# Kernel tuning notes

Hardware: AMD Instinct MI355X
Metric: run time of the kernel (lower is better)

The kernel has to match this reference:

```python
import jax, jax.numpy as jnp
import numpy as np

U = 128          # uniform segment extent (operand_extent)
NSEG = 32        # segments per operand (in0, in1, out)
NPATH = 512      # number of paths
BATCH = 2048


def setup_inputs() -> dict:
    key = jax.random.key(0)
    k0, k1, kc, kp0, kp1, kpo = jax.random.split(key, 6)
    x0 = jax.random.normal(k0, (BATCH, NSEG * U), dtype=jnp.float32)
    x1 = jax.random.normal(k1, (BATCH, NSEG * U), dtype=jnp.float32)
    coeffs = jax.random.normal(kc, (NPATH,), dtype=jnp.float32)
    p0 = jax.random.randint(kp0, (NPATH,), 0, NSEG, dtype=jnp.int32)
    p1 = jax.random.randint(kp1, (NPATH,), 0, NSEG, dtype=jnp.int32)
    pout = jax.random.randint(kpo, (NPATH,), 0, NSEG, dtype=jnp.int32)
    return {"x0": x0, "x1": x1, "coeffs": coeffs, "p0": p0, "p1": p1, "pout": pout}


def reference(x0, x1, coeffs, p0, p1, pout):
    # Segmented uniform tensor product, subscripts 'u,u,u':
    # out[b, pout[k], :] += coeffs[k] * x0[b, p0[k], :] * x1[b, p1[k], :]
    B = x0.shape[0]
    x0s = x0.reshape(B, NSEG, U)
    x1s = x1.reshape(B, NSEG, U)
    # gather per-path segments: [B, P, U]
    contrib = x0s[:, p0, :] * x1s[:, p1, :] * coeffs[None, :, None]
    out = jnp.zeros((B, NSEG, U), dtype=x0.dtype).at[:, pout, :].add(contrib)
    return out.reshape(B, NSEG * U)
```

## Files before the change

### kernel.cpp

```cpp
#include <hip/hip_runtime.h>

#define U 128
#define NSEG 32
#define NPATH 512
#define ROW (NSEG * U)
#define NW 8

struct Meta { unsigned pp; float c; };
struct WS {
    Meta meta[NPATH];
    int  segstart[NSEG + 1];
    int  wsplit[NW + 1];
};

__global__ __launch_bounds__(512) void build_csr(const float* __restrict__ coeffs,
                                                 const int* __restrict__ p0,
                                                 const int* __restrict__ p1,
                                                 const int* __restrict__ pout,
                                                 WS* __restrict__ ws) {
    __shared__ int wcnt[NPATH / 64][NSEG];
    __shared__ int wpre[NPATH / 64][NSEG];
    __shared__ int sseg[NSEG + 1];
    __shared__ int stot[NSEG];

    const int k    = threadIdx.x;
    const int lane = k & 63;
    const int wave = k >> 6;

    const int   po = pout[k];
    const int   a0 = p0[k];
    const int   a1 = p1[k];
    const float c  = coeffs[k];

    const unsigned long long lt = (1ull << lane) - 1ull;
    int rank = 0;
    #pragma unroll
    for (int s = 0; s < NSEG; ++s) {
        unsigned long long m = __ballot(po == s);
        if (po == s)  rank = (int)__popcll(m & lt);
        if (lane == s) wcnt[wave][s] = (int)__popcll(m);
    }
    __syncthreads();

    if (k < NSEG) {
        int tot = 0;
        #pragma unroll
        for (int w = 0; w < NPATH / 64; ++w) { wpre[w][k] = tot; tot += wcnt[w][k]; }
        stot[k] = tot;
    }
    __syncthreads();

    if (k < 64) {
        int v = (k < NSEG) ? stot[k] : 0;
        int inc = v;
        #pragma unroll
        for (int d = 1; d < 64; d <<= 1) {
            int t = __shfl_up(inc, d, 64);
            if (k >= d) inc += t;
        }
        int excl = inc - v;
        if (k < NSEG) sseg[k] = excl;
        if (k == NSEG - 1) sseg[NSEG] = excl + v;
    }
    __syncthreads();

    {
        Meta m;
        m.pp = (unsigned)a0 | ((unsigned)a1 << 16);
        m.c  = c;
        ws->meta[sseg[po] + wpre[wave][po] + rank] = m;
    }
    if (k <= NSEG) ws->segstart[k] = sseg[k];

    if (k < 64) {
        #pragma unroll
        for (int w = 1; w < NW; ++w) {
            const int target = (NPATH * w) / NW;
            int key;
            if (k <= NSEG) {
                int d = sseg[k] - target; if (d < 0) d = -d;
                key = (d << 6) | k;
            } else key = 0x7fffffff;
            #pragma unroll
            for (int m = 32; m >= 1; m >>= 1) {
                int o = __shfl_xor(key, m, 64);
                key = (o < key) ? o : key;
            }
            if (k == 0) ws->wsplit[w] = key & 63;
        }
        if (k == 0) { ws->wsplit[0] = 0; ws->wsplit[NW] = NSEG; }
    }
}

__global__ __launch_bounds__(512) void tp_kernel(const float* __restrict__ x0,
                                                 const float* __restrict__ x1,
                                                 const WS* __restrict__ ws,
                                                 float* __restrict__ out) {
    __shared__ float lds0[ROW];
    __shared__ float lds1[ROW];
    __shared__ Meta  smeta[NPATH];
    __shared__ int   sseg[NSEG + 1];
    __shared__ int   ssplit[NW + 1];

    const int b   = blockIdx.x;
    const int tid = threadIdx.x;

    const float4* g0 = reinterpret_cast<const float4*>(x0 + (size_t)b * ROW);
    const float4* g1 = reinterpret_cast<const float4*>(x1 + (size_t)b * ROW);
    float4* s0v = reinterpret_cast<float4*>(lds0);
    float4* s1v = reinterpret_cast<float4*>(lds1);
    #pragma unroll
    for (int j = 0; j < (ROW / 4) / 512; ++j) {
        s0v[tid + j * 512] = g0[tid + j * 512];
        s1v[tid + j * 512] = g1[tid + j * 512];
    }
    if (tid < NPATH / 2)
        reinterpret_cast<float4*>(smeta)[tid] =
            reinterpret_cast<const float4*>(ws->meta)[tid];
    if (tid < NSEG + 1) sseg[tid] = ws->segstart[tid];
    if (tid < NW + 1)   ssplit[tid] = ws->wsplit[tid];
    __syncthreads();

    const int wave = tid >> 6;
    const int lane = tid & 63;
    const int half = lane >> 5;
    const int sub  = lane & 31;

    const int sBeg = __builtin_amdgcn_readfirstlane(ssplit[wave]);
    const int sEnd = __builtin_amdgcn_readfirstlane(ssplit[wave + 1]);

    const float4* s0q = reinterpret_cast<const float4*>(lds0);
    const float4* s1q = reinterpret_cast<const float4*>(lds1);
    float* outrow = out + (size_t)b * ROW;

    for (int s = sBeg; s < sEnd; ++s) {
        const int jb = __builtin_amdgcn_readfirstlane(sseg[s]);
        const int je = __builtin_amdgcn_readfirstlane(sseg[s + 1]);
        float4 acc0 = make_float4(0.f, 0.f, 0.f, 0.f);
        float4 acc1 = make_float4(0.f, 0.f, 0.f, 0.f);
        int j = jb;
        for (; j + 3 < je; j += 4) {
            const Meta mA = smeta[j + half];
            const Meta mB = smeta[j + 2 + half];
            const float4 uA = s0q[(mA.pp & 0xffffu) * (U / 4) + sub];
            const float4 wA = s1q[(mA.pp >> 16)     * (U / 4) + sub];
            const float4 uB = s0q[(mB.pp & 0xffffu) * (U / 4) + sub];
            const float4 wB = s1q[(mB.pp >> 16)     * (U / 4) + sub];
            acc0.x += mA.c * uA.x * wA.x;
            acc0.y += mA.c * uA.y * wA.y;
            acc0.z += mA.c * uA.z * wA.z;
            acc0.w += mA.c * uA.w * wA.w;
            acc1.x += mB.c * uB.x * wB.x;
            acc1.y += mB.c * uB.y * wB.y;
            acc1.z += mB.c * uB.z * wB.z;
            acc1.w += mB.c * uB.w * wB.w;
        }
        for (; j + 1 < je; j += 2) {
            const Meta m = smeta[j + half];
            const float4 u = s0q[(m.pp & 0xffffu) * (U / 4) + sub];
            const float4 w = s1q[(m.pp >> 16)     * (U / 4) + sub];
            acc0.x += m.c * u.x * w.x;
            acc0.y += m.c * u.y * w.y;
            acc0.z += m.c * u.z * w.z;
            acc0.w += m.c * u.w * w.w;
        }
        if (j < je) {
            const Meta m = smeta[j];
            const float cc = (half == 0) ? m.c : 0.f;
            const float4 u = s0q[(m.pp & 0xffffu) * (U / 4) + sub];
            const float4 w = s1q[(m.pp >> 16)     * (U / 4) + sub];
            acc0.x += cc * u.x * w.x;
            acc0.y += cc * u.y * w.y;
            acc0.z += cc * u.z * w.z;
            acc0.w += cc * u.w * w.w;
        }
        float4 a;
        a.x = acc0.x + acc1.x;
        a.y = acc0.y + acc1.y;
        a.z = acc0.z + acc1.z;
        a.w = acc0.w + acc1.w;
        a.x += __shfl_xor(a.x, 32, 64);
        a.y += __shfl_xor(a.y, 32, 64);
        a.z += __shfl_xor(a.z, 32, 64);
        a.w += __shfl_xor(a.w, 32, 64);
        if (half == 0)
            reinterpret_cast<float4*>(outrow + s * U)[sub] = a;
    }
}

extern "C" void kernel_launch(void* const* d_in, const int* in_sizes, int n_in,
                              void* d_out, int out_size, void* d_ws, size_t ws_size,
                              hipStream_t stream) {
    const float* x0     = (const float*)d_in[0];
    const float* x1     = (const float*)d_in[1];
    const float* coeffs = (const float*)d_in[2];
    const int*   p0     = (const int*)d_in[3];
    const int*   p1     = (const int*)d_in[4];
    const int*   pout   = (const int*)d_in[5];
    float* out = (float*)d_out;
    WS* ws = (WS*)d_ws;

    build_csr<<<1, 512, 0, stream>>>(coeffs, p0, p1, pout, ws);
    tp_kernel<<<2048, 512, 0, stream>>>(x0, x1, ws, out);
}
```

Baseline: 36.40 us.

## Process four rows per block with double-buffered async global-to-LDS prefetch

Each block now handles four batch rows instead of one, and the grid is cut to a quarter of its former size. While the current row is computed, the next row's x0/x1 segments are prefetched straight into a second LDS buffer using global_load_lds. The aim is to hide global-load latency behind compute and to amortise the per-block metadata load. In exchange, LDS per block roughly doubles, which lowers the number of resident blocks per CU. The grid is also small relative to the CU count, so there are fewer waves to hide latency.

```diff
diff --git a/kernel.cpp b/kernel.cpp
--- a/kernel.cpp
+++ b/kernel.cpp
@@ -5,6 +5,8 @@
 #define NPATH 512
 #define ROW (NSEG * U)
 #define NW 8
+#define ROWS_PER_BLOCK 4
+#define NBLK 512
 
 struct Meta { unsigned pp; float c; };
 struct WS {
@@ -12,6 +14,11 @@
     int  segstart[NSEG + 1];
     int  wsplit[NW + 1];
 };
+
+typedef __attribute__((address_space(1))) const void gl_void;
+typedef __attribute__((address_space(3))) void       lds_void;
+#define GLOAD_LDS16(g, l)                                                  \
+    __builtin_amdgcn_global_load_lds((gl_void*)(g), (lds_void*)(l), 16, 0, 0)
 
 __global__ __launch_bounds__(512) void build_csr(const float* __restrict__ coeffs,
                                                  const int* __restrict__ p0,
@@ -96,23 +103,23 @@
                                                  const float* __restrict__ x1,
                                                  const WS* __restrict__ ws,
                                                  float* __restrict__ out) {
-    __shared__ float lds0[ROW];
-    __shared__ float lds1[ROW];
-    __shared__ Meta  smeta[NPATH];
-    __shared__ int   sseg[NSEG + 1];
-    __shared__ int   ssplit[NW + 1];
-
-    const int b   = blockIdx.x;
+    __shared__ __align__(16) float lbuf[2][2 * ROW];
+    __shared__ Meta smeta[NPATH];
+    __shared__ int  sseg[NSEG + 1];
+    __shared__ int  ssplit[NW + 1];
+
     const int tid = threadIdx.x;
-
-    const float4* g0 = reinterpret_cast<const float4*>(x0 + (size_t)b * ROW);
-    const float4* g1 = reinterpret_cast<const float4*>(x1 + (size_t)b * ROW);
-    float4* s0v = reinterpret_cast<float4*>(lds0);
-    float4* s1v = reinterpret_cast<float4*>(lds1);
-    #pragma unroll
-    for (int j = 0; j < (ROW / 4) / 512; ++j) {
-        s0v[tid + j * 512] = g0[tid + j * 512];
-        s1v[tid + j * 512] = g1[tid + j * 512];
+    const int b0  = blockIdx.x * ROWS_PER_BLOCK;
+
+    {
+        const float* r0 = x0 + (size_t)b0 * ROW;
+        const float* r1 = x1 + (size_t)b0 * ROW;
+        #pragma unroll
+        for (int c = 0; c < 2; ++c) {
+            const int e = (c * 512 + tid) * 4;
+            GLOAD_LDS16(r0 + e, &lbuf[0][e]);
+            GLOAD_LDS16(r1 + e, &lbuf[0][ROW + e]);
+        }
     }
     if (tid < NPATH / 2)
         reinterpret_cast<float4*>(smeta)[tid] =
@@ -129,62 +136,77 @@
     const int sBeg = __builtin_amdgcn_readfirstlane(ssplit[wave]);
     const int sEnd = __builtin_amdgcn_readfirstlane(ssplit[wave + 1]);
 
-    const float4* s0q = reinterpret_cast<const float4*>(lds0);
-    const float4* s1q = reinterpret_cast<const float4*>(lds1);
-    float* outrow = out + (size_t)b * ROW;
-
-    for (int s = sBeg; s < sEnd; ++s) {
-        const int jb = __builtin_amdgcn_readfirstlane(sseg[s]);
-        const int je = __builtin_amdgcn_readfirstlane(sseg[s + 1]);
-        float4 acc0 = make_float4(0.f, 0.f, 0.f, 0.f);
-        float4 acc1 = make_float4(0.f, 0.f, 0.f, 0.f);
-        int j = jb;
-        for (; j + 3 < je; j += 4) {
-            const Meta mA = smeta[j + half];
-            const Meta mB = smeta[j + 2 + half];
-            const float4 uA = s0q[(mA.pp & 0xffffu) * (U / 4) + sub];
-            const float4 wA = s1q[(mA.pp >> 16)     * (U / 4) + sub];
-            const float4 uB = s0q[(mB.pp & 0xffffu) * (U / 4) + sub];
-            const float4 wB = s1q[(mB.pp >> 16)     * (U / 4) + sub];
-            acc0.x += mA.c * uA.x * wA.x;
-            acc0.y += mA.c * uA.y * wA.y;
-            acc0.z += mA.c * uA.z * wA.z;
-            acc0.w += mA.c * uA.w * wA.w;
-            acc1.x += mB.c * uB.x * wB.x;
-            acc1.y += mB.c * uB.y * wB.y;
-            acc1.z += mB.c * uB.z * wB.z;
-            acc1.w += mB.c * uB.w * wB.w;
-        }
-        for (; j + 1 < je; j += 2) {
-            const Meta m = smeta[j + half];
-            const float4 u = s0q[(m.pp & 0xffffu) * (U / 4) + sub];
-            const float4 w = s1q[(m.pp >> 16)     * (U / 4) + sub];
-            acc0.x += m.c * u.x * w.x;
-            acc0.y += m.c * u.y * w.y;
-            acc0.z += m.c * u.z * w.z;
-            acc0.w += m.c * u.w * w.w;
-        }
-        if (j < je) {
-            const Meta m = smeta[j];
-            const float cc = (half == 0) ? m.c : 0.f;
-            const float4 u = s0q[(m.pp & 0xffffu) * (U / 4) + sub];
-            const float4 w = s1q[(m.pp >> 16)     * (U / 4) + sub];
-            acc0.x += cc * u.x * w.x;
-            acc0.y += cc * u.y * w.y;
-            acc0.z += cc * u.z * w.z;
-            acc0.w += cc * u.w * w.w;
-        }
-        float4 a;
-        a.x = acc0.x + acc1.x;
-        a.y = acc0.y + acc1.y;
-        a.z = acc0.z + acc1.z;
-        a.w = acc0.w + acc1.w;
-        a.x += __shfl_xor(a.x, 32, 64);
-        a.y += __shfl_xor(a.y, 32, 64);
-        a.z += __shfl_xor(a.z, 32, 64);
-        a.w += __shfl_xor(a.w, 32, 64);
-        if (half == 0)
-            reinterpret_cast<float4*>(outrow + s * U)[sub] = a;
+    for (int r = 0; r < ROWS_PER_BLOCK; ++r) {
+        const int cur = r & 1;
+        if (r + 1 < ROWS_PER_BLOCK) {
+            const float* r0 = x0 + (size_t)(b0 + r + 1) * ROW;
+            const float* r1 = x1 + (size_t)(b0 + r + 1) * ROW;
+            #pragma unroll
+            for (int c = 0; c < 2; ++c) {
+                const int e = (c * 512 + tid) * 4;
+                GLOAD_LDS16(r0 + e, &lbuf[cur ^ 1][e]);
+                GLOAD_LDS16(r1 + e, &lbuf[cur ^ 1][ROW + e]);
+            }
+        }
+
+        const float4* s0q = reinterpret_cast<const float4*>(&lbuf[cur][0]);
+        const float4* s1q = reinterpret_cast<const float4*>(&lbuf[cur][ROW]);
+        float* outrow = out + (size_t)(b0 + r) * ROW;
+
+        for (int s = sBeg; s < sEnd; ++s) {
+            const int jb = __builtin_amdgcn_readfirstlane(sseg[s]);
+            const int je = __builtin_amdgcn_readfirstlane(sseg[s + 1]);
+            float4 acc0 = make_float4(0.f, 0.f, 0.f, 0.f);
+            float4 acc1 = make_float4(0.f, 0.f, 0.f, 0.f);
+            int j = jb;
+            for (; j + 3 < je; j += 4) {
+                const Meta mA = smeta[j + half];
+                const Meta mB = smeta[j + 2 + half];
+                const float4 uA = s0q[(mA.pp & 0xffffu) * (U / 4) + sub];
+                const float4 wA = s1q[(mA.pp >> 16)     * (U / 4) + sub];
+                const float4 uB = s0q[(mB.pp & 0xffffu) * (U / 4) + sub];
+                const float4 wB = s1q[(mB.pp >> 16)     * (U / 4) + sub];
+                acc0.x += mA.c * uA.x * wA.x;
+                acc0.y += mA.c * uA.y * wA.y;
+                acc0.z += mA.c * uA.z * wA.z;
+                acc0.w += mA.c * uA.w * wA.w;
+                acc1.x += mB.c * uB.x * wB.x;
+                acc1.y += mB.c * uB.y * wB.y;
+                acc1.z += mB.c * uB.z * wB.z;
+                acc1.w += mB.c * uB.w * wB.w;
+            }
+            for (; j + 1 < je; j += 2) {
+                const Meta m = smeta[j + half];
+                const float4 u = s0q[(m.pp & 0xffffu) * (U / 4) + sub];
+                const float4 w = s1q[(m.pp >> 16)     * (U / 4) + sub];
+                acc0.x += m.c * u.x * w.x;
+                acc0.y += m.c * u.y * w.y;
+                acc0.z += m.c * u.z * w.z;
+                acc0.w += m.c * u.w * w.w;
+            }
+            if (j < je) {
+                const Meta m = smeta[j];
+                const float cc = (half == 0) ? m.c : 0.f;
+                const float4 u = s0q[(m.pp & 0xffffu) * (U / 4) + sub];
+                const float4 w = s1q[(m.pp >> 16)     * (U / 4) + sub];
+                acc0.x += cc * u.x * w.x;
+                acc0.y += cc * u.y * w.y;
+                acc0.z += cc * u.z * w.z;
+                acc0.w += cc * u.w * w.w;
+            }
+            float4 a;
+            a.x = acc0.x + acc1.x;
+            a.y = acc0.y + acc1.y;
+            a.z = acc0.z + acc1.z;
+            a.w = acc0.w + acc1.w;
+            a.x += __shfl_xor(a.x, 32, 64);
+            a.y += __shfl_xor(a.y, 32, 64);
+            a.z += __shfl_xor(a.z, 32, 64);
+            a.w += __shfl_xor(a.w, 32, 64);
+            if (half == 0)
+                reinterpret_cast<float4*>(outrow + s * U)[sub] = a;
+        }
+        __syncthreads();
     }
 }
 
@@ -201,5 +223,5 @@
     WS* ws = (WS*)d_ws;
 
     build_csr<<<1, 512, 0, stream>>>(coeffs, p0, p1, pout, ws);
-    tp_kernel<<<2048, 512, 0, stream>>>(x0, x1, ws, out);
+    tp_kernel<<<NBLK, 512, 0, stream>>>(x0, x1, ws, out);
 }
```

Measured after the change: 37.81 us. 1.04x slower.
